# Optimization experiments

Hardware: AMD Instinct MI355X
Metric: run time of the kernel (lower is better)

## Reference

```python
import jax, jax.numpy as jnp
import numpy as np

NUM_HEADS = 8
EPS = 1e-5

def layer_norm(x, g, b):
    m = jnp.mean(x, axis=-1, keepdims=True)
    v = jnp.mean(jnp.square(x - m), axis=-1, keepdims=True)
    return (x - m) * jax.lax.rsqrt(v + EPS) * g + b

def setup_inputs() -> dict:
    key = jax.random.key(0)
    ks = jax.random.split(key, 16)
    B, C_enc, C_dec = 2, 512, 256
    H = W = D = 16
    d_ff = 4 * C_dec
    s = 0.02
    inp = {
        'encoder_feat': jax.random.normal(ks[0], (B, C_enc, H, W, D), jnp.float32),
        'decoder_feat': jax.random.normal(ks[1], (B, C_dec, H, W, D), jnp.float32),
        # projections stored as (in, out)
        'Wq': jax.random.normal(ks[2], (C_dec, C_dec), jnp.float32) * s,
        'bq': jnp.zeros((C_dec,), jnp.float32),
        'Wk': jax.random.normal(ks[3], (C_enc, C_dec), jnp.float32) * s,
        'bk': jnp.zeros((C_dec,), jnp.float32),
        'Wv': jax.random.normal(ks[4], (C_enc, C_dec), jnp.float32) * s,
        'bv': jnp.zeros((C_dec,), jnp.float32),
        'Wo': jax.random.normal(ks[5], (C_dec, C_dec), jnp.float32) * s,
        'bo': jnp.zeros((C_dec,), jnp.float32),
        'g_enc': jnp.ones((C_enc,), jnp.float32),
        'b_enc': jnp.zeros((C_enc,), jnp.float32),
        'g_dec': jnp.ones((C_dec,), jnp.float32),
        'b_dec': jnp.zeros((C_dec,), jnp.float32),
        'g_out': jnp.ones((C_dec,), jnp.float32),
        'b_out': jnp.zeros((C_dec,), jnp.float32),
        'W1': jax.random.normal(ks[6], (C_dec, d_ff), jnp.float32) * s,
        'b1': jnp.zeros((d_ff,), jnp.float32),
        'W2': jax.random.normal(ks[7], (d_ff, C_dec), jnp.float32) * s,
        'b2': jnp.zeros((C_dec,), jnp.float32),
    }
    return inp

def reference(encoder_feat, decoder_feat, Wq, bq, Wk, bk, Wv, bv, Wo, bo,
              g_enc, b_enc, g_dec, b_dec, g_out, b_out, W1, b1, W2, b2):
    B, C_dec, H, W, D = decoder_feat.shape
    h = NUM_HEADS
    hd = C_dec // h
    scale = hd ** -0.5
    # flatten spatial dims -> sequences [B, S, C]
    enc_seq = encoder_feat.reshape(B, encoder_feat.shape[1], -1).transpose(0, 2, 1)
    dec_seq = decoder_feat.reshape(B, C_dec, -1).transpose(0, 2, 1)
    enc_n = layer_norm(enc_seq, g_enc, b_enc)
    dec_n = layer_norm(dec_seq, g_dec, b_dec)
    Sq = dec_n.shape[1]
    Sk = enc_n.shape[1]
    Q = (dec_n @ Wq + bq).reshape(B, Sq, h, hd).transpose(0, 2, 1, 3)
    K = (enc_n @ Wk + bk).reshape(B, Sk, h, hd).transpose(0, 2, 1, 3)
    V = (enc_n @ Wv + bv).reshape(B, Sk, h, hd).transpose(0, 2, 1, 3)
    attn = jnp.einsum('bhqd,bhkd->bhqk', Q, K) * scale
    attn = jax.nn.softmax(attn, axis=-1)
    out = jnp.einsum('bhqk,bhkd->bhqd', attn, V)
    out = out.transpose(0, 2, 1, 3).reshape(B, Sq, C_dec)
    out = out @ Wo + bo
    out = dec_seq + out
    ffn = jax.nn.gelu(layer_norm(out, g_out, b_out) @ W1 + b1, approximate=False) @ W2 + b2
    out = out + ffn
    return out.transpose(0, 2, 1).reshape(B, C_dec, H, W, D)
```

## Files before the change

kernel.cpp:

```cpp
#include <hip/hip_runtime.h>
#include <hip/hip_bf16.h>
#include <math.h>
#include <stdint.h>

typedef __hip_bfloat16 bf16;
typedef __attribute__((ext_vector_type(8))) short short8;
typedef __attribute__((ext_vector_type(4))) short short4v;
typedef __attribute__((ext_vector_type(4))) float f32x4;

#define B_   2
#define S_   4096
#define CE   512
#define CD   256
#define DFF  1024
#define NH   8
#define HD   32

static __device__ __forceinline__ float b2f(bf16 x) { return __bfloat162float(x); }
static __device__ __forceinline__ bf16  f2b(float x) { return __float2bfloat16(x); }
static __device__ __forceinline__ short f2bs(float x) {
  bf16 h = f2b(x); return __builtin_bit_cast(short, h);
}
static __device__ __forceinline__ float s2f(short x) {
  return b2f(__builtin_bit_cast(bf16, x));
}
static __device__ __forceinline__ bool is_f32(const unsigned* graw) {
  return graw[0] == 0x3F800000u;
}

static __device__ __forceinline__ float exp2_(float x) {
#if __has_builtin(__builtin_amdgcn_exp2f)
  return __builtin_amdgcn_exp2f(x);
#else
  float r; asm("v_exp_f32 %0, %1" : "=v"(r) : "v"(x)); return r;
#endif
}
static __device__ __forceinline__ unsigned cvt_pk_bf16(float lo, float hi) {
  unsigned r;
  asm("v_cvt_pk_bf16_f32 %0, %1, %2" : "=v"(r) : "v"(lo), "v"(hi));
  return r;
}

#define GLD16(gptr, lptr) \
  __builtin_amdgcn_global_load_lds( \
      (const __attribute__((address_space(1))) unsigned int*)(gptr), \
      (__attribute__((address_space(3))) unsigned int*)(lptr), 16, 0, 0)

#define WAITVM(N) asm volatile("s_waitcnt vmcnt(" #N ")" ::: "memory")
#define BAR() __builtin_amdgcn_s_barrier()

struct PrepTab {
  const void* tsrc[6];
  bf16* tdst[6];
  int tK[6], tsStr[6], tdStr[6];
  float tscl[6];
  int tbase[7];
  const void* csrc[14];
  bf16* cdst[14];
  float cscl[14];
  int coff[15];
};

__global__ __launch_bounds__(256) void prep_kernel(
    PrepTab p, const unsigned* __restrict__ graw) {
  __shared__ bf16 tile[32][33];
  bool f32i = is_f32(graw);
  int blk = blockIdx.x;
  if (blk < p.tbase[6]) {
    int j = 0;
    #pragma unroll 1
    while (blk >= p.tbase[j + 1]) ++j;
    int local = blk - p.tbase[j];
    int ktiles = p.tK[j] >> 5;
    int nt = local / ktiles, kt = local - nt * ktiles;
    int k0 = kt * 32, n0 = nt * 32;
    const void* src = p.tsrc[j];
    bf16* dst = p.tdst[j];
    int sStr = p.tsStr[j], dStr = p.tdStr[j];
    float scl = p.tscl[j];
    int t = threadIdx.x;
    int tc = t & 31, tr = t >> 5;
    #pragma unroll
    for (int i = 0; i < 32; i += 8) {
      size_t idx = (size_t)(k0 + tr + i) * sStr + n0 + tc;
      float v = f32i ? ((const float*)src)[idx] : b2f(((const bf16*)src)[idx]);
      tile[tr + i][tc] = f2b(v * scl);
    }
    __syncthreads();
    #pragma unroll
    for (int i = 0; i < 32; i += 8)
      dst[(size_t)(n0 + tr + i) * dStr + k0 + tc] = tile[tc][tr + i];
  } else {
    int idx = (blk - p.tbase[6]) * 256 + threadIdx.x;
    int e4 = idx * 4;
    if (e4 >= p.coff[14]) return;
    int j = 0;
    #pragma unroll 1
    while (e4 >= p.coff[j + 1]) ++j;
    int local = e4 - p.coff[j];
    float v0, v1, v2, v3;
    if (f32i) {
      float4 f = *(const float4*)((const float*)p.csrc[j] + local);
      v0 = f.x; v1 = f.y; v2 = f.z; v3 = f.w;
    } else {
      short4v h = *(const short4v*)((const short*)p.csrc[j] + local);
      v0 = s2f(h[0]); v1 = s2f(h[1]); v2 = s2f(h[2]); v3 = s2f(h[3]);
    }
    float scl = p.cscl[j];
    short4v o;
    o[0] = f2bs(v0 * scl); o[1] = f2bs(v1 * scl);
    o[2] = f2bs(v2 * scl); o[3] = f2bs(v3 * scl);
    *(short4v*)((short*)p.cdst[j] + local) = o;
  }
}

struct LNCfg {
  const bf16 *x, *g, *bt;
  bf16 *xn, *xt;
  int C;
};

template<int CC, bool XT>
static __device__ __forceinline__ void ln_tile_body(
    const LNCfg& T, int b, int s0, short* sT, short* sG, short* sBt) {
  constexpr int P = CC + 8;
  constexpr int NJ = CC / 64;
  int t = threadIdx.x;
  if (t < CC / 8)      *(short8*)&sG[t * 8] = ((const short8*)T.g)[t];
  else if (t < CC / 4) *(short8*)&sBt[(t - CC/8) * 8] = ((const short8*)T.bt)[t - CC/8];

  int cg = t >> 2;
  int sq = (t & 3) * 8;
  const short* xg = (const short*)T.x + (size_t)b * CC * S_ + s0 + sq;
  short8 ld[NJ];
  #pragma unroll
  for (int ci = 0; ci < NJ; ++ci)
    ld[ci] = *(const short8*)(xg + (size_t)(ci * 64 + cg) * S_);
  #pragma unroll
  for (int ci = 0; ci < NJ; ++ci) {
    int c = ci * 64 + cg;
    #pragma unroll
    for (int j = 0; j < 8; ++j) {
      int s = sq + j;
      sT[s * P + (c ^ ((s & 24) << 1))] = ld[ci][j];
    }
  }
  __syncthreads();

  int w = t >> 6, l = t & 63;
  int grp = l >> 3, k = l & 7;
  int s = w * 8 + grp;
  int Z = (s & 24) << 1;
  short8 vals[NJ];
  float sum = 0.f, sq2 = 0.f;
  #pragma unroll
  for (int j = 0; j < NJ; ++j) {
    vals[j] = *(const short8*)&sT[s * P + j * 64 + ((k * 8) ^ Z)];
    #pragma unroll
    for (int i = 0; i < 8; ++i) {
      float v = s2f(vals[j][i]);
      sum += v; sq2 += v * v;
    }
  }
  #pragma unroll
  for (int off = 1; off < 8; off <<= 1) {
    sum += __shfl_xor(sum, off);
    sq2 += __shfl_xor(sq2, off);
  }
  float mean = sum * (1.f / CC);
  float rstd = rsqrtf(sq2 * (1.f / CC) - mean * mean + 1e-5f);
  size_t ro = ((size_t)b * S_ + s0 + s) * CC;
  #pragma unroll
  for (int j = 0; j < NJ; ++j) {
    int c0 = j * 64 + k * 8;
    short8 gv = *(const short8*)&sG[c0];
    short8 bv = *(const short8*)&sBt[c0];
    short8 o;
    #pragma unroll
    for (int i = 0; i < 8; ++i) {
      float v = s2f(vals[j][i]);
      o[i] = f2bs((v - mean) * rstd * s2f(gv[i]) + s2f(bv[i]));
    }
    *(short8*)((short*)T.xn + ro + c0) = o;
    if (XT) *(short8*)((short*)T.xt + ro + c0) = vals[j];
  }
}

__global__ __launch_bounds__(256) void ln_tile_kernel(LNCfg e, LNCfg d) {
  __shared__ __align__(16) short sT[32 * 520];
  __shared__ __align__(16) short sG[512], sBt[512];
  int gb = blockIdx.x;
  int local = gb & 255;
  int b = local >> 7, s0 = (local & 127) * 32;
  if (gb < 256) ln_tile_body<512, false>(e, b, s0, sT, sG, sBt);
  else          ln_tile_body<256, true>(d, b, s0, sT, sG, sBt);
}

__global__ __launch_bounds__(256) void ln_rows_kernel(
    const float* __restrict__ x, const bf16* __restrict__ g,
    const bf16* __restrict__ bt, bf16* __restrict__ xn, int C) {
  int wave = threadIdx.x >> 6, lane = threadIdx.x & 63;
  int row = blockIdx.x * 4 + wave;
  float4 v = *(const float4*)(x + (size_t)row * 256 + lane * 4);
  float sum = v.x + v.y + v.z + v.w;
  float sq = v.x * v.x + v.y * v.y + v.z * v.z + v.w * v.w;
  #pragma unroll
  for (int off = 1; off < 64; off <<= 1) {
    sum += __shfl_xor(sum, off);
    sq  += __shfl_xor(sq, off);
  }
  float mean = sum * (1.f / 256.f);
  float rstd = rsqrtf(sq * (1.f / 256.f) - mean * mean + 1e-5f);
  short4v gg = *(const short4v*)((const short*)g + lane * 4);
  short4v bb = *(const short4v*)((const short*)bt + lane * 4);
  short4v o;
  o[0] = f2bs((v.x - mean) * rstd * s2f(gg[0]) + s2f(bb[0]));
  o[1] = f2bs((v.y - mean) * rstd * s2f(gg[1]) + s2f(bb[1]));
  o[2] = f2bs((v.z - mean) * rstd * s2f(gg[2]) + s2f(bb[2]));
  o[3] = f2bs((v.w - mean) * rstd * s2f(gg[3]) + s2f(bb[3]));
  *(short4v*)((short*)xn + (size_t)row * 256 + lane * 4) = o;
}

__global__ __launch_bounds__(256) void gemm_mfma_kernel(
    const bf16* __restrict__ A, const bf16* __restrict__ Wt,
    const bf16* __restrict__ bias, int M, int N, int K,
    const bf16* __restrict__ resid_bf, const float* __restrict__ resid_f,
    bf16* __restrict__ out_bf, float* __restrict__ out_f,
    void* __restrict__ out_t, const unsigned* __restrict__ graw,
    int act, int resid_mode, int out_mode) {
  __shared__ __align__(16) short sA[3][128 * 32];
  __shared__ __align__(16) short sB[3][64 * 32];
  int m0 = blockIdx.y * 128, n0 = blockIdx.x * 64;
  int t = threadIdx.x;
  int w = t >> 6;
  int wm = w >> 1, wn = w & 1;
  int n16 = t & 15, quad = (t & 63) >> 4;
  int srow = t >> 2, skg = (t & 3) * 8;

  f32x4 acc[4][2] = {};
  const short* Ag = (const short*)A;
  const short* Wg = (const short*)Wt;
  const short* a0p = Ag + (size_t)(m0 + srow) * K + skg;
  const short* a1p = Ag + (size_t)(m0 + 64 + srow) * K + skg;
  const short* wp  = Wg + (size_t)(n0 + srow) * K + skg;

  auto stage = [&](int buf, int kk) {
    GLD16(a0p + kk, (char*)sA[buf] + t * 16);
    GLD16(a1p + kk, (char*)sA[buf] + t * 16 + 4096);
    GLD16(wp + kk,  (char*)sB[buf] + t * 16);
  };
  int nt = K >> 5;
  stage(0, 0);
  stage(1, 32);
  WAITVM(3);
  BAR();

  for (int ti = 0; ti < nt; ++ti) {
    int cur = ti % 3;
    bool pf = (ti + 2) < nt;
    if (pf) stage((ti + 2) % 3, (ti + 2) * 32);
    short8 af[4], bfr[2];
    #pragma unroll
    for (int ms = 0; ms < 4; ++ms)
      af[ms] = *(const short8*)&sA[cur][(wm * 64 + ms * 16 + n16) * 32 + quad * 8];
    #pragma unroll
    for (int ns = 0; ns < 2; ++ns)
      bfr[ns] = *(const short8*)&sB[cur][(wn * 32 + ns * 16 + n16) * 32 + quad * 8];
    #pragma unroll
    for (int ms = 0; ms < 4; ++ms)
      #pragma unroll
      for (int ns = 0; ns < 2; ++ns)
        acc[ms][ns] = __builtin_amdgcn_mfma_f32_16x16x32_bf16(
            af[ms], bfr[ns], acc[ms][ns], 0, 0, 0);
    if (pf) WAITVM(3); else WAITVM(0);
    BAR();
  }

  #pragma unroll
  for (int ms = 0; ms < 4; ++ms) {
    #pragma unroll
    for (int ns = 0; ns < 2; ++ns) {
      int col = n0 + wn * 32 + ns * 16 + n16;
      float bv = b2f(bias[col]);
      #pragma unroll
      for (int r = 0; r < 4; ++r) {
        int row = m0 + wm * 64 + ms * 16 + quad * 4 + r;
        float c = acc[ms][ns][r] + bv;
        if (act == 1) c = 0.5f * c * (1.f + erff(c * 0.70710678118654752f));
        size_t off = (size_t)row * N + col;
        if (resid_mode == 1)      c += b2f(resid_bf[off]);
        else if (resid_mode == 2) c += resid_f[off];
        if (out_f) out_f[off] = c;
        else       out_bf[off] = f2b(c);
      }
    }
  }
}

__global__ __launch_bounds__(256) void gemm64_mfma_kernel(
    const bf16* __restrict__ A, const bf16* __restrict__ Wt,
    const bf16* __restrict__ bias, int M, int N, int K,
    const bf16* __restrict__ resid_bf, const float* __restrict__ resid_f,
    bf16* __restrict__ out_bf, float* __restrict__ out_f,
    void* __restrict__ out_t, const unsigned* __restrict__ graw,
    int act, int resid_mode, int out_mode) {
  __shared__ __align__(16) short sA[3][64 * 32];
  __shared__ __align__(16) short sB[3][64 * 32];
  int m0 = blockIdx.y * 64, n0 = blockIdx.x * 64;
  int t = threadIdx.x;
  int w = t >> 6;
  int wm = w >> 1, wn = w & 1;
  int n16 = t & 15, quad = (t & 63) >> 4;
  int srow = t >> 2, skg = (t & 3) * 8;

  f32x4 acc[2][2] = {};
  const short* Ag = (const short*)A;
  const short* Wg = (const short*)Wt;
  const short* ap = Ag + (size_t)(m0 + srow) * K + skg;
  const short* wp = Wg + (size_t)(n0 + srow) * K + skg;

  auto stage = [&](int buf, int kk) {
    GLD16(ap + kk, (char*)sA[buf] + t * 16);
    GLD16(wp + kk, (char*)sB[buf] + t * 16);
  };
  int nt = K >> 5;
  stage(0, 0);
  stage(1, 32);
  WAITVM(2);
  BAR();

  for (int ti = 0; ti < nt; ++ti) {
    int cur = ti % 3;
    bool pf = (ti + 2) < nt;
    if (pf) stage((ti + 2) % 3, (ti + 2) * 32);
    short8 af[2], bfr[2];
    #pragma unroll
    for (int ms = 0; ms < 2; ++ms)
      af[ms] = *(const short8*)&sA[cur][(wm * 32 + ms * 16 + n16) * 32 + quad * 8];
    #pragma unroll
    for (int ns = 0; ns < 2; ++ns)
      bfr[ns] = *(const short8*)&sB[cur][(wn * 32 + ns * 16 + n16) * 32 + quad * 8];
    #pragma unroll
    for (int ms = 0; ms < 2; ++ms)
      #pragma unroll
      for (int ns = 0; ns < 2; ++ns)
        acc[ms][ns] = __builtin_amdgcn_mfma_f32_16x16x32_bf16(
            af[ms], bfr[ns], acc[ms][ns], 0, 0, 0);
    if (pf) WAITVM(2); else WAITVM(0);
    BAR();
  }

  if (out_mode == 3) {
    bool isf32 = is_f32(graw);
    #pragma unroll
    for (int ms = 0; ms < 2; ++ms) {
      int row0 = m0 + wm * 32 + ms * 16 + quad * 4;
      int bb = row0 >> 12, s = row0 & (S_ - 1);
      #pragma unroll
      for (int ns = 0; ns < 2; ++ns) {
        int col = n0 + wn * 32 + ns * 16 + n16;
        float bv = b2f(bias[col]);
        float cv[4];
        #pragma unroll
        for (int r = 0; r < 4; ++r)
          cv[r] = acc[ms][ns][r] + bv + resid_f[(size_t)(row0 + r) * N + col];
        size_t oidx = ((size_t)bb * CD + col) * S_ + s;
        if (isf32) {
          float4 v4 = {cv[0], cv[1], cv[2], cv[3]};
          *(float4*)((float*)out_t + oidx) = v4;
        } else {
          short4v v;
          #pragma unroll
          for (int r = 0; r < 4; ++r) v[r] = f2bs(cv[r]);
          *(short4v*)((bf16*)out_t + oidx) = v;
        }
      }
    }
    return;
  }

  #pragma unroll
  for (int ms = 0; ms < 2; ++ms) {
    #pragma unroll
    for (int ns = 0; ns < 2; ++ns) {
      int col = n0 + wn * 32 + ns * 16 + n16;
      float bv = b2f(bias[col]);
      #pragma unroll
      for (int r = 0; r < 4; ++r) {
        int row = m0 + wm * 32 + ms * 16 + quad * 4 + r;
        float c = acc[ms][ns][r] + bv;
        if (act == 1) c = 0.5f * c * (1.f + erff(c * 0.70710678118654752f));
        size_t off = (size_t)row * N + col;
        if (resid_mode == 1)      c += b2f(resid_bf[off]);
        else if (resid_mode == 2) c += resid_f[off];
        if (out_f) out_f[off] = c;
        else       out_bf[off] = f2b(c);
      }
    }
  }
}

__global__ __launch_bounds__(256) void qkv_kernel(
    const bf16* __restrict__ dec_n, const bf16* __restrict__ enc_n,
    const bf16* __restrict__ Wqt, const bf16* __restrict__ Wkvt,
    const bf16* __restrict__ bq, const bf16* __restrict__ bkv,
    bf16* __restrict__ Qm, bf16* __restrict__ Km, bf16* __restrict__ VT) {
  __shared__ __align__(16) short sA[3][64 * 32];
  __shared__ __align__(16) short sB[3][64 * 32];
  bool isQ = blockIdx.x < 4;
  const short* Ag = (const short*)(isQ ? dec_n : enc_n);
  const short* Wg = (const short*)(isQ ? Wqt : Wkvt);
  const bf16* bias = isQ ? bq : bkv;
  int K = isQ ? CD : CE;
  int n0 = isQ ? blockIdx.x * 64 : (blockIdx.x - 4) * 64;
  int m0 = blockIdx.y * 64;
  int t = threadIdx.x;
  int w = t >> 6;
  int wm = w >> 1, wn = w & 1;
  int n16 = t & 15, quad = (t & 63) >> 4;
  int srow = t >> 2, skg = (t & 3) * 8;

  f32x4 acc[2][2] = {};
  const short* ap = Ag + (size_t)(m0 + srow) * K + skg;
  const short* wp = Wg + (size_t)(n0 + srow) * K + skg;
  auto stage = [&](int buf, int kk) {
    GLD16(ap + kk, (char*)sA[buf] + t * 16);
    GLD16(wp + kk, (char*)sB[buf] + t * 16);
  };
  int nt = K >> 5;
  stage(0, 0);
  stage(1, 32);
  WAITVM(2);
  BAR();

  for (int ti = 0; ti < nt; ++ti) {
    int cur = ti % 3;
    bool pf = (ti + 2) < nt;
    if (pf) stage((ti + 2) % 3, (ti + 2) * 32);
    short8 af[2], bfr[2];
    #pragma unroll
    for (int ms = 0; ms < 2; ++ms)
      af[ms] = *(const short8*)&sA[cur][(wm * 32 + ms * 16 + n16) * 32 + quad * 8];
    #pragma unroll
    for (int ns = 0; ns < 2; ++ns)
      bfr[ns] = *(const short8*)&sB[cur][(wn * 32 + ns * 16 + n16) * 32 + quad * 8];
    #pragma unroll
    for (int ms = 0; ms < 2; ++ms)
      #pragma unroll
      for (int ns = 0; ns < 2; ++ns)
        acc[ms][ns] = __builtin_amdgcn_mfma_f32_16x16x32_bf16(
            af[ms], bfr[ns], acc[ms][ns], 0, 0, 0);
    if (pf) WAITVM(2); else WAITVM(0);
    BAR();
  }

  if (!isQ && n0 >= 256) {
    #pragma unroll
    for (int ms = 0; ms < 2; ++ms) {
      int row0 = m0 + wm * 32 + ms * 16 + quad * 4;
      int bb = row0 >> 12, s = row0 & (S_ - 1);
      #pragma unroll
      for (int ns = 0; ns < 2; ++ns) {
        int col = n0 + wn * 32 + ns * 16 + n16;
        float bv = b2f(bias[col]);
        short4v v;
        #pragma unroll
        for (int r = 0; r < 4; ++r) v[r] = f2bs(acc[ms][ns][r] + bv);
        *(short4v*)(VT + ((size_t)bb * CD + col - 256) * S_ + s) = v;
      }
    }
    return;
  }
  bf16* outp = isQ ? Qm : Km;
  #pragma unroll
  for (int ms = 0; ms < 2; ++ms) {
    #pragma unroll
    for (int ns = 0; ns < 2; ++ns) {
      int col = n0 + wn * 32 + ns * 16 + n16;
      float bv = b2f(bias[col]);
      #pragma unroll
      for (int r = 0; r < 4; ++r) {
        int row = m0 + wm * 32 + ms * 16 + quad * 4 + r;
        outp[(size_t)row * CD + col] = f2b(acc[ms][ns][r] + bv);
      }
    }
  }
}

__global__ __launch_bounds__(256) void attn_mfma_kernel(
    const bf16* __restrict__ Qm, const bf16* __restrict__ Km,
    const bf16* __restrict__ VT, float* __restrict__ Op0,
    float* __restrict__ Op1, float* __restrict__ Lp) {
  __shared__ __align__(16) short sKf[2][4][64][8];
  __shared__ __align__(16) short sVt[2][32][64];
  __shared__ __align__(16) short sP[4][16][72];
  int b = blockIdx.z, h = blockIdx.y >> 1, half = blockIdx.y & 1;
  int q0 = blockIdx.x * 64;
  int t = threadIdx.x;
  int w = t >> 6, l = t & 63;
  int n = l & 15, quad = l >> 4;
  size_t bh = ((size_t)b * S_) * CD + h * HD;
  const short* vtg = (const short*)VT +
      (size_t)(b * CD + h * HD + w * 8 + (l >> 3)) * S_ + ((l & 7) ^ ((l >> 3) & 7)) * 8;
  const short* kg = (const short*)Km + bh + (size_t)(w * 16 + n) * CD + quad * 8;

  short8 qf = *(const short8*)((const short*)Qm + bh +
                               (size_t)(q0 + w * 16 + n) * CD + quad * 8);
  short8 ones8;
  #pragma unroll
  for (int i = 0; i < 8; ++i) ones8[i] = (short)0x3F80;

  f32x4 o0 = {0.f, 0.f, 0.f, 0.f}, o1 = {0.f, 0.f, 0.f, 0.f};
  f32x4 ol = {0.f, 0.f, 0.f, 0.f};

  auto stageKV = [&](int buf, int kk) {
    GLD16(kg + (size_t)kk * CD, &sKf[buf][w][l][0]);
    GLD16(vtg + kk, (short*)sVt[buf] + w * 512 + l * 8);
  };

  int kbeg = half * (S_ / 2), kend = kbeg + S_ / 2;
  stageKV(0, kbeg);
  WAITVM(0);
  BAR();
  int cur = 0;
  for (int k0 = kbeg; k0 < kend; k0 += 64) {
    if (k0 + 64 < kend) stageKV(cur ^ 1, k0 + 64);

    f32x4 sc[4];
    #pragma unroll
    for (int st = 0; st < 4; ++st) {
      short8 kf = *(const short8*)&sKf[cur][st][l][0];
      f32x4 z = {0.f, 0.f, 0.f, 0.f};
      sc[st] = __builtin_amdgcn_mfma_f32_16x16x32_bf16(kf, qf, z, 0, 0, 0);
    }
    #pragma unroll
    for (int st = 0; st < 4; ++st) {
      float e0 = exp2_(sc[st][0]);
      float e1 = exp2_(sc[st][1]);
      float e2 = exp2_(sc[st][2]);
      float e3 = exp2_(sc[st][3]);
      unsigned w01 = cvt_pk_bf16(e0, e1);
      unsigned w23 = cvt_pk_bf16(e2, e3);
      *(int2*)&sP[w][n][st * 16 + quad * 4] = make_int2((int)w01, (int)w23);
    }
    #pragma unroll
    for (int kc = 0; kc < 2; ++kc) {
      int p8 = (kc * 4 + quad) ^ (n & 7);
      short8 pf = *(const short8*)&sP[w][n][kc * 32 + quad * 8];
      short8 v0 = *(const short8*)&sVt[cur][n][p8 * 8];
      short8 v1 = *(const short8*)&sVt[cur][16 + n][p8 * 8];
      o0 = __builtin_amdgcn_mfma_f32_16x16x32_bf16(pf, v0, o0, 0, 0, 0);
      o1 = __builtin_amdgcn_mfma_f32_16x16x32_bf16(pf, v1, o1, 0, 0, 0);
      ol = __builtin_amdgcn_mfma_f32_16x16x32_bf16(pf, ones8, ol, 0, 0, 0);
    }
    WAITVM(0);
    BAR();
    cur ^= 1;
  }

  float* Opb = half ? Op1 : Op0;
  size_t pb = (size_t)b * S_;
  #pragma unroll
  for (int r = 0; r < 4; ++r) {
    int q = q0 + w * 16 + quad * 4 + r;
    float* orow = Opb + (pb + q) * CD + h * HD;
    orow[n]      = o0[r];
    orow[16 + n] = o1[r];
    if (n == 0) Lp[((size_t)(b * 2 + half) * S_ + q) * NH + h] = ol[r];
  }
}

__global__ __launch_bounds__(256) void attn_combine_kernel(
    const float* __restrict__ Op0, const float* __restrict__ Op1,
    const float* __restrict__ Lp, bf16* __restrict__ Am) {
  int idx = blockIdx.x * 256 + threadIdx.x;
  int c = (idx * 4) & (CD - 1);
  int bs = (idx * 4) >> 8;
  int s = bs & (S_ - 1), b = bs >> 12;
  int h = c >> 5;
  size_t row = (size_t)b * S_ + s;
  float l0 = Lp[((size_t)(b * 2 + 0) * S_ + s) * NH + h];
  float l1 = Lp[((size_t)(b * 2 + 1) * S_ + s) * NH + h];
  float inv = 1.f / (l0 + l1);
  float4 a = *(const float4*)&Op0[row * CD + c];
  float4 d = *(const float4*)&Op1[row * CD + c];
  short4v v;
  v[0] = f2bs((a.x + d.x) * inv);
  v[1] = f2bs((a.y + d.y) * inv);
  v[2] = f2bs((a.z + d.z) * inv);
  v[3] = f2bs((a.w + d.w) * inv);
  *(short4v*)&Am[row * CD + c] = v;
}

extern "C" void kernel_launch(void* const* d_in, const int* in_sizes, int n_in,
                              void* d_out, int out_size, void* d_ws, size_t ws_size,
                              hipStream_t stream) {
  const float kscale = 0.25503486f;
  const unsigned* graw = (const unsigned*)d_in[10];
  char* base = (char*)d_ws;
  size_t pos = 256;

  auto alloc = [&](size_t bytes) {
    char* p = base + pos; pos = (pos + bytes + 255) & ~(size_t)255; return p;
  };
  int cidx[14] = {0, 1, 3, 5, 7, 9, 10, 11, 12, 13, 14, 15, 17, 19};
  bf16* conv[20] = {};
  for (int k = 0; k < 14; ++k) {
    int i = cidx[k];
    conv[i] = (bf16*)alloc((size_t)2 * in_sizes[i]);
  }
  bf16* Wqt  = (bf16*)alloc((size_t)CD * CD * 2);
  bf16* Wkvt = (bf16*)alloc((size_t)CE * CE * 2);
  bf16* Wot  = (bf16*)alloc((size_t)CD * CD * 2);
  bf16* W1t  = (bf16*)alloc((size_t)DFF * CD * 2);
  bf16* W2t  = (bf16*)alloc((size_t)CD * DFF * 2);
  bf16* bkv  = (bf16*)alloc((size_t)CE * 2);
  conv[5] = bkv;
  conv[7] = bkv + CD;

  bf16*  enc_n = (bf16*) alloc((size_t)B_ * S_ * CE * 2);
  bf16*  dec_n = (bf16*) alloc((size_t)B_ * S_ * CD * 2);
  bf16*  Qm    = (bf16*) alloc((size_t)B_ * S_ * CD * 2);
  bf16*  Km    = (bf16*) alloc((size_t)B_ * S_ * CD * 2);
  bf16*  VT    = (bf16*) alloc((size_t)B_ * S_ * CD * 2);
  float* outm  = (float*)alloc((size_t)B_ * S_ * CD * 4);
  bf16*  hid   = (bf16*) alloc((size_t)B_ * S_ * DFF * 2);
  float* Lp    = (float*)alloc((size_t)B_ * 2 * S_ * NH * 4);
  bf16*  Am    = dec_n;
  bf16*  ln2   = Km;
  bf16*  dec_t = (bf16*)hid;
  float* Op0   = outm;
  float* Op1   = (float*)enc_n;

  PrepTab p;
  p.tsrc[0] = d_in[2];  p.tdst[0] = Wqt;            p.tK[0] = CD;  p.tsStr[0] = CD;  p.tdStr[0] = CD;  p.tscl[0] = kscale;
  p.tsrc[1] = d_in[4];  p.tdst[1] = Wkvt;           p.tK[1] = CE;  p.tsStr[1] = CD;  p.tdStr[1] = CE;  p.tscl[1] = 1.0f;
  p.tsrc[2] = d_in[6];  p.tdst[2] = Wkvt + CD * CE; p.tK[2] = CE;  p.tsStr[2] = CD;  p.tdStr[2] = CE;  p.tscl[2] = 1.0f;
  p.tsrc[3] = d_in[8];  p.tdst[3] = Wot;            p.tK[3] = CD;  p.tsStr[3] = CD;  p.tdStr[3] = CD;  p.tscl[3] = 1.0f;
  p.tsrc[4] = d_in[16]; p.tdst[4] = W1t;            p.tK[4] = CD;  p.tsStr[4] = DFF; p.tdStr[4] = CD;  p.tscl[4] = 1.0f;
  p.tsrc[5] = d_in[18]; p.tdst[5] = W2t;            p.tK[5] = DFF; p.tsStr[5] = CD;  p.tdStr[5] = DFF; p.tscl[5] = 1.0f;
  int tN[6] = {CD, CD, CD, CD, DFF, CD};
  p.tbase[0] = 0;
  for (int j = 0; j < 6; ++j)
    p.tbase[j + 1] = p.tbase[j] + (tN[j] / 32) * (p.tK[j] / 32);
  int coff = 0;
  for (int k = 0; k < 14; ++k) {
    int i = cidx[k];
    p.csrc[k] = d_in[i];
    p.cdst[k] = conv[i];
    p.cscl[k] = (i == 3) ? kscale : 1.0f;
    p.coff[k] = coff;
    coff += in_sizes[i];
  }
  p.coff[14] = coff;
  int prep_blocks = p.tbase[6] + (coff / 4 + 255) / 256;

  const bf16* enc_c = conv[0];
  const bf16* dec_c = conv[1];
  const bf16 *bq_c = conv[3], *bo_c = conv[9];
  const bf16 *ge_c = conv[10], *be_c = conv[11];
  const bf16 *gd_c = conv[12], *bd_c = conv[13];
  const bf16 *go_c = conv[14], *bo2_c = conv[15];
  const bf16 *b1_c = conv[17], *b2_c = conv[19];

  const int M = B_ * S_;

  prep_kernel<<<prep_blocks, 256, 0, stream>>>(p, graw);

  LNCfg lne = {enc_c, ge_c, be_c, enc_n, nullptr, CE};
  LNCfg lnd = {dec_c, gd_c, bd_c, dec_n, dec_t, CD};
  ln_tile_kernel<<<512, 256, 0, stream>>>(lne, lnd);

  qkv_kernel<<<dim3(12, M / 64), 256, 0, stream>>>(
      dec_n, enc_n, Wqt, Wkvt, bq_c, bkv, Qm, Km, VT);

  attn_mfma_kernel<<<dim3(S_ / 64, NH * 2, B_), 256, 0, stream>>>(Qm, Km, VT, Op0, Op1, Lp);
  attn_combine_kernel<<<(M * CD / 4) / 256, 256, 0, stream>>>(Op0, Op1, Lp, Am);

  gemm64_mfma_kernel<<<dim3(CD / 64, M / 64), 256, 0, stream>>>(
      Am, Wot, bo_c, M, CD, CD, dec_t, nullptr, nullptr, outm, nullptr, graw, 0, 1, 0);

  ln_rows_kernel<<<dim3(M / 4), 256, 0, stream>>>(outm, go_c, bo2_c, ln2, CD);

  gemm_mfma_kernel<<<dim3(DFF / 64, M / 128), 256, 0, stream>>>(
      ln2, W1t, b1_c, M, DFF, CD, nullptr, nullptr, hid, nullptr, nullptr, graw, 1, 0, 0);
  gemm64_mfma_kernel<<<dim3(CD / 64, M / 64), 256, 0, stream>>>(
      hid, W2t, b2_c, M, CD, DFF, nullptr, outm, nullptr, nullptr, d_out, graw, 0, 0, 3);
}
```

Before: 257.5 us.

## Keep softmax P in registers via permlane swaps and load V directly from global

Removes the LDS round-trip for the probability matrix P. The exp results are rearranged across lanes with permlane32/16 swap instructions so they form the MFMA A-operand directly. V is now read straight from global memory into registers each iteration instead of being staged through LDS, and s_setprio brackets are placed around the MFMA groups. This cuts LDS traffic and shared memory use, at the cost of exposed global-load latency for V, which is no longer prefetched a tile ahead.

```diff
diff --git a/kernel.cpp b/kernel.cpp
--- a/kernel.cpp
+++ b/kernel.cpp
@@ -7,6 +7,8 @@
 typedef __attribute__((ext_vector_type(8))) short short8;
 typedef __attribute__((ext_vector_type(4))) short short4v;
 typedef __attribute__((ext_vector_type(4))) float f32x4;
+typedef __attribute__((ext_vector_type(4))) unsigned int uint32x4;
+typedef __attribute__((ext_vector_type(2))) unsigned int uint32x2;
 
 #define B_   2
 #define S_   4096
@@ -39,6 +41,22 @@
   unsigned r;
   asm("v_cvt_pk_bf16_f32 %0, %1, %2" : "=v"(r) : "v"(lo), "v"(hi));
   return r;
+}
+static __device__ __forceinline__ void perm32(unsigned& a, unsigned& b) {
+#if __has_builtin(__builtin_amdgcn_permlane32_swap)
+  uint32x2 r = __builtin_amdgcn_permlane32_swap(a, b, false, false);
+  a = r[0]; b = r[1];
+#else
+  asm("v_permlane32_swap_b32 %0, %1" : "+v"(a), "+v"(b));
+#endif
+}
+static __device__ __forceinline__ void perm16(unsigned& a, unsigned& b) {
+#if __has_builtin(__builtin_amdgcn_permlane16_swap)
+  uint32x2 r = __builtin_amdgcn_permlane16_swap(a, b, false, false);
+  a = r[0]; b = r[1];
+#else
+  asm("v_permlane16_swap_b32 %0, %1" : "+v"(a), "+v"(b));
+#endif
 }
 
 #define GLD16(gptr, lptr) \
@@ -492,17 +510,14 @@
     const bf16* __restrict__ VT, float* __restrict__ Op0,
     float* __restrict__ Op1, float* __restrict__ Lp) {
   __shared__ __align__(16) short sKf[2][4][64][8];
-  __shared__ __align__(16) short sVt[2][32][64];
-  __shared__ __align__(16) short sP[4][16][72];
   int b = blockIdx.z, h = blockIdx.y >> 1, half = blockIdx.y & 1;
   int q0 = blockIdx.x * 64;
   int t = threadIdx.x;
   int w = t >> 6, l = t & 63;
   int n = l & 15, quad = l >> 4;
   size_t bh = ((size_t)b * S_) * CD + h * HD;
-  const short* vtg = (const short*)VT +
-      (size_t)(b * CD + h * HD + w * 8 + (l >> 3)) * S_ + ((l & 7) ^ ((l >> 3) & 7)) * 8;
   const short* kg = (const short*)Km + bh + (size_t)(w * 16 + n) * CD + quad * 8;
+  const short* vg = (const short*)VT + (size_t)(b * CD + h * HD + n) * S_ + quad * 8;
 
   short8 qf = *(const short8*)((const short*)Qm + bh +
                                (size_t)(q0 + w * 16 + n) * CD + quad * 8);
@@ -513,46 +528,59 @@
   f32x4 o0 = {0.f, 0.f, 0.f, 0.f}, o1 = {0.f, 0.f, 0.f, 0.f};
   f32x4 ol = {0.f, 0.f, 0.f, 0.f};
 
-  auto stageKV = [&](int buf, int kk) {
-    GLD16(kg + (size_t)kk * CD, &sKf[buf][w][l][0]);
-    GLD16(vtg + kk, (short*)sVt[buf] + w * 512 + l * 8);
-  };
-
   int kbeg = half * (S_ / 2), kend = kbeg + S_ / 2;
-  stageKV(0, kbeg);
+  GLD16(kg + (size_t)kbeg * CD, &sKf[0][w][l][0]);
   WAITVM(0);
   BAR();
   int cur = 0;
   for (int k0 = kbeg; k0 < kend; k0 += 64) {
-    if (k0 + 64 < kend) stageKV(cur ^ 1, k0 + 64);
+    if (k0 + 64 < kend)
+      GLD16(kg + (size_t)(k0 + 64) * CD, &sKf[cur ^ 1][w][l][0]);
+
+    const short* vb = vg + k0;
+    short8 v00 = *(const short8*)(vb);
+    short8 v01 = *(const short8*)(vb + 32);
+    short8 v10 = *(const short8*)(vb + (size_t)16 * S_);
+    short8 v11 = *(const short8*)(vb + (size_t)16 * S_ + 32);
 
     f32x4 sc[4];
+    __builtin_amdgcn_s_setprio(1);
     #pragma unroll
     for (int st = 0; st < 4; ++st) {
       short8 kf = *(const short8*)&sKf[cur][st][l][0];
       f32x4 z = {0.f, 0.f, 0.f, 0.f};
       sc[st] = __builtin_amdgcn_mfma_f32_16x16x32_bf16(kf, qf, z, 0, 0, 0);
     }
+    __builtin_amdgcn_s_setprio(0);
+
+    unsigned Wd[4][2];
     #pragma unroll
     for (int st = 0; st < 4; ++st) {
-      float e0 = exp2_(sc[st][0]);
-      float e1 = exp2_(sc[st][1]);
-      float e2 = exp2_(sc[st][2]);
-      float e3 = exp2_(sc[st][3]);
-      unsigned w01 = cvt_pk_bf16(e0, e1);
-      unsigned w23 = cvt_pk_bf16(e2, e3);
-      *(int2*)&sP[w][n][st * 16 + quad * 4] = make_int2((int)w01, (int)w23);
-    }
-    #pragma unroll
-    for (int kc = 0; kc < 2; ++kc) {
-      int p8 = (kc * 4 + quad) ^ (n & 7);
-      short8 pf = *(const short8*)&sP[w][n][kc * 32 + quad * 8];
-      short8 v0 = *(const short8*)&sVt[cur][n][p8 * 8];
-      short8 v1 = *(const short8*)&sVt[cur][16 + n][p8 * 8];
-      o0 = __builtin_amdgcn_mfma_f32_16x16x32_bf16(pf, v0, o0, 0, 0, 0);
-      o1 = __builtin_amdgcn_mfma_f32_16x16x32_bf16(pf, v1, o1, 0, 0, 0);
-      ol = __builtin_amdgcn_mfma_f32_16x16x32_bf16(pf, ones8, ol, 0, 0, 0);
-    }
+      Wd[st][0] = cvt_pk_bf16(exp2_(sc[st][0]), exp2_(sc[st][1]));
+      Wd[st][1] = cvt_pk_bf16(exp2_(sc[st][2]), exp2_(sc[st][3]));
+    }
+    uint32x4 pw0, pw1;
+    #pragma unroll
+    for (int m = 0; m < 2; ++m) {
+      unsigned a0 = Wd[0][m], b0 = Wd[1][m];
+      perm32(a0, b0); perm16(a0, b0);
+      pw0[m] = a0; pw0[2 + m] = b0;
+      unsigned a1 = Wd[2][m], b1 = Wd[3][m];
+      perm32(a1, b1); perm16(a1, b1);
+      pw1[m] = a1; pw1[2 + m] = b1;
+    }
+    short8 pf0 = __builtin_bit_cast(short8, pw0);
+    short8 pf1 = __builtin_bit_cast(short8, pw1);
+
+    __builtin_amdgcn_s_setprio(1);
+    o0 = __builtin_amdgcn_mfma_f32_16x16x32_bf16(pf0, v00, o0, 0, 0, 0);
+    o1 = __builtin_amdgcn_mfma_f32_16x16x32_bf16(pf0, v10, o1, 0, 0, 0);
+    ol = __builtin_amdgcn_mfma_f32_16x16x32_bf16(pf0, ones8, ol, 0, 0, 0);
+    o0 = __builtin_amdgcn_mfma_f32_16x16x32_bf16(pf1, v01, o0, 0, 0, 0);
+    o1 = __builtin_amdgcn_mfma_f32_16x16x32_bf16(pf1, v11, o1, 0, 0, 0);
+    ol = __builtin_amdgcn_mfma_f32_16x16x32_bf16(pf1, ones8, ol, 0, 0, 0);
+    __builtin_amdgcn_s_setprio(0);
+
     WAITVM(0);
     BAR();
     cur ^= 1;
```

Result: slower. 359.3 us (+39.5%).
